# Kernel optimization log

Hardware: AMD Instinct MI355X
Metric: run time of the kernel (lower is better)

Reference implementation:

```python
import jax, jax.numpy as jnp
import numpy as np

N_NODES = 100000
N_EDGES = 3200000
IN_FEAT = 512
HIDDEN = 64
N_GRAPHS = 2048


def setup_inputs() -> dict:
    key = jax.random.key(0)
    ks = jax.random.split(key, 8)
    x = jax.random.normal(ks[0], (N_NODES, IN_FEAT), dtype=jnp.float32)
    edge_index = jax.random.randint(ks[1], (2, N_EDGES), 0, N_NODES, dtype=jnp.int64)
    batch = jnp.sort(jax.random.randint(ks[2], (N_NODES,), 0, N_GRAPHS, dtype=jnp.int64))
    W1 = jax.random.normal(ks[3], (IN_FEAT, HIDDEN), dtype=jnp.float32) * (1.0 / np.sqrt(IN_FEAT))
    b1 = jnp.zeros((HIDDEN,), dtype=jnp.float32)
    W2 = jax.random.normal(ks[4], (HIDDEN, HIDDEN), dtype=jnp.float32) * (1.0 / np.sqrt(HIDDEN))
    b2 = jnp.zeros((HIDDEN,), dtype=jnp.float32)
    fc_w = jax.random.normal(ks[5], (HIDDEN, 1), dtype=jnp.float32) * (1.0 / np.sqrt(HIDDEN))
    fc_b = jnp.zeros((1,), dtype=jnp.float32)
    return {"x": x, "edge_index": edge_index, "batch": batch, "num_graphs": N_GRAPHS,
            "W1": W1, "b1": b1, "W2": W2, "b2": b2, "fc_w": fc_w, "fc_b": fc_b}


def _gcn_conv(x, src, dst, n_nodes, W, b):
    # PyG GCNConv: h = X W; out = D^{-1/2}(A+I)D^{-1/2} h + b  (self-loops already in src/dst)
    h = x @ W  # [N, out]
    ones = jnp.ones_like(src, dtype=h.dtype)
    deg = jax.ops.segment_sum(ones, dst, num_segments=n_nodes)  # in-degree incl. self-loop
    dinv = jnp.where(deg > 0, jax.lax.rsqrt(deg), 0.0)
    norm = dinv[src] * dinv[dst]  # [E+N]
    msgs = h[src] * norm[:, None]  # gather + scale
    out = jax.ops.segment_sum(msgs, dst, num_segments=n_nodes)  # scatter-add
    return out + b


def reference(x, edge_index, batch, num_graphs, W1, b1, W2, b2, fc_w, fc_b):
    n = x.shape[0]
    loops = jnp.arange(n, dtype=edge_index.dtype)
    src = jnp.concatenate([edge_index[0], loops])
    dst = jnp.concatenate([edge_index[1], loops])

    h = jax.nn.relu(_gcn_conv(x, src, dst, n, W1, b1))
    h = _gcn_conv(h, src, dst, n, W2, b2)

    # global_mean_pool over graph ids
    sums = jax.ops.segment_sum(h, batch, num_segments=num_graphs)
    cnts = jax.ops.segment_sum(jnp.ones((n,), dtype=h.dtype), batch, num_segments=num_graphs)
    pooled = sums / jnp.maximum(cnts, 1.0)[:, None]
    return pooled @ fc_w + fc_b  # [num_graphs, 1]
```

## Files before the change

### kernel.cpp

```cpp
#include <hip/hip_runtime.h>
#include <hip/hip_bf16.h>

#define N_NODES  100000
#define N_EDGES  3200000
#define IN_FEAT  512
#define HIDDEN   64
#define N_GRAPHS 2048

typedef __attribute__((ext_vector_type(8))) short short8;
typedef __attribute__((ext_vector_type(4))) float floatx4;

__global__ __launch_bounds__(256) void zero_u32(unsigned* __restrict__ p, int n) {
    int i = blockIdx.x * 256 + threadIdx.x;
    if (i < n) p[i] = 0u;
}

__global__ __launch_bounds__(256) void init_deg(int* __restrict__ degi, int n) {
    int i = blockIdx.x * 256 + threadIdx.x;
    if (i < n) degi[i] = 1;
}

__global__ __launch_bounds__(256) void deg_rank(const int* __restrict__ dst,
                                                int* __restrict__ degi,
                                                int* __restrict__ rank, int e) {
    int i = (blockIdx.x * 256 + threadIdx.x) * 4;
    if (i + 4 <= e) {
        int4 d = *(const int4*)(dst + i);
        int4 r;
        r.x = atomicAdd(&degi[d.x], 1);
        r.y = atomicAdd(&degi[d.y], 1);
        r.z = atomicAdd(&degi[d.z], 1);
        r.w = atomicAdd(&degi[d.w], 1);
        *(int4*)(rank + i) = r;
    } else {
        for (int j = i; j < e; j++) rank[j] = atomicAdd(&degi[dst[j]], 1);
    }
}

__global__ __launch_bounds__(256) void compute_dinv(const int* __restrict__ degi,
                                                    float* __restrict__ dinv, int n) {
    int i = blockIdx.x * 256 + threadIdx.x;
    if (i < n) dinv[i] = 1.0f / sqrtf((float)degi[i]);
}

__global__ __launch_bounds__(256) void count_graphs(const int* __restrict__ batch,
                                                    int* __restrict__ cntg, int n) {
    int i = blockIdx.x * 256 + threadIdx.x;
    if (i < n) atomicAdd(&cntg[batch[i]], 1);
}

#define SCAN_CHUNK 2048

__global__ __launch_bounds__(256) void scan_block_sums(const int* __restrict__ degi,
                                                       int* __restrict__ bsums, int n) {
    __shared__ int sdata[256];
    int t = threadIdx.x;
    int base = blockIdx.x * SCAN_CHUNK;
    int s = 0;
    for (int i = 0; i < 8; i++) {
        int idx = base + t * 8 + i;
        if (idx < n) s += degi[idx] - 1;
    }
    sdata[t] = s;
    __syncthreads();
    for (int off = 128; off > 0; off >>= 1) {
        if (t < off) sdata[t] += sdata[t + off];
        __syncthreads();
    }
    if (t == 0) bsums[blockIdx.x] = sdata[0];
}

__global__ void scan_bsums(int* __restrict__ bsums, int nb) {
    if (blockIdx.x == 0 && threadIdx.x == 0) {
        int acc = 0;
        for (int i = 0; i < nb; i++) { int v = bsums[i]; bsums[i] = acc; acc += v; }
    }
}

__global__ __launch_bounds__(256) void scan_write(const int* __restrict__ degi,
                                                  const int* __restrict__ bsums,
                                                  int* __restrict__ row_start, int n) {
    __shared__ int sthread[256];
    int t = threadIdx.x;
    int base = blockIdx.x * SCAN_CHUNK;
    int local[8];
    int s = 0;
    for (int i = 0; i < 8; i++) {
        int idx = base + t * 8 + i;
        int c = (idx < n) ? (degi[idx] - 1) : 0;
        local[i] = s;
        s += c;
    }
    sthread[t] = s;
    __syncthreads();
    for (int off = 1; off < 256; off <<= 1) {
        int v = (t >= off) ? sthread[t - off] : 0;
        __syncthreads();
        sthread[t] += v;
        __syncthreads();
    }
    int off0 = bsums[blockIdx.x] + sthread[t] - s;
    for (int i = 0; i < 8; i++) {
        int idx = base + t * 8 + i;
        if (idx < n) row_start[idx] = off0 + local[i];
    }
}

__global__ __launch_bounds__(256) void csr_scatter(const int* __restrict__ src,
                                                   const int* __restrict__ dst,
                                                   const int* __restrict__ rank,
                                                   const int* __restrict__ rowst,
                                                   int* __restrict__ csr_src, int e) {
    int i = (blockIdx.x * 256 + threadIdx.x) * 4;
    if (i + 4 <= e) {
        int4 d = *(const int4*)(dst + i);
        int4 s = *(const int4*)(src + i);
        int4 r = *(const int4*)(rank + i);
        csr_src[rowst[d.x] + r.x - 1] = s.x;
        csr_src[rowst[d.y] + r.y - 1] = s.y;
        csr_src[rowst[d.z] + r.z - 1] = s.z;
        csr_src[rowst[d.w] + r.w - 1] = s.w;
    } else {
        for (int j = i; j < e; j++)
            csr_src[rowst[dst[j]] + rank[j] - 1] = src[j];
    }
}

__device__ inline void bf16_split(float f, short& hi, short& lo) {
    unsigned u = __float_as_uint(f);
    unsigned r = (u + 0x7fffu + ((u >> 16) & 1u)) >> 16;
    float fh = __uint_as_float(r << 16);
    float fl = f - fh;
    unsigned v = __float_as_uint(fl);
    unsigned s = (v + 0x7fffu + ((v >> 16) & 1u)) >> 16;
    hi = (short)r;
    lo = (short)s;
}

template <int K>
__global__ __launch_bounds__(256) void gemm_mfma(const float* __restrict__ X,
                                                 const float* __restrict__ W,
                                                 const float* __restrict__ dinv,
                                                 float* __restrict__ Y, int nrows) {
    constexpr int BSTR = 40;
    __shared__ short bhi[64 * BSTR];
    __shared__ short blo[64 * BSTR];

    const int t    = threadIdx.x;
    const int wave = t >> 6;
    const int lane = t & 63;
    const int quad = lane >> 4;
    const int l16  = lane & 15;

    const int arow   = blockIdx.x * 64 + wave * 16 + l16;
    const bool rvalid = arow < nrows;
    const float* xrow = X + (size_t)arow * K;

    const int scol = t & 63;
    const int skg  = t >> 6;

    floatx4 acc[4] = {};

#pragma unroll 1
    for (int k0 = 0; k0 < K; k0 += 32) {
        float wv[8];
#pragma unroll
        for (int j = 0; j < 8; j++)
            wv[j] = W[(size_t)(k0 + skg * 8 + j) * 64 + scol];
        short8 whi, wlo;
#pragma unroll
        for (int j = 0; j < 8; j++) { short h, l; bf16_split(wv[j], h, l); whi[j] = h; wlo[j] = l; }

        __syncthreads();
        *(short8*)&bhi[scol * BSTR + skg * 8] = whi;
        *(short8*)&blo[scol * BSTR + skg * 8] = wlo;

        float av[8] = {0.f, 0.f, 0.f, 0.f, 0.f, 0.f, 0.f, 0.f};
        if (rvalid) {
            float4 p0 = *(const float4*)(xrow + k0 + quad * 8);
            float4 p1 = *(const float4*)(xrow + k0 + quad * 8 + 4);
            av[0] = p0.x; av[1] = p0.y; av[2] = p0.z; av[3] = p0.w;
            av[4] = p1.x; av[5] = p1.y; av[6] = p1.z; av[7] = p1.w;
        }
        short8 ahi, alo;
#pragma unroll
        for (int j = 0; j < 8; j++) { short h, l; bf16_split(av[j], h, l); ahi[j] = h; alo[j] = l; }

        __syncthreads();

#pragma unroll
        for (int ct = 0; ct < 4; ct++) {
            int col = ct * 16 + l16;
            short8 bh = *(short8*)&bhi[col * BSTR + quad * 8];
            short8 bl = *(short8*)&blo[col * BSTR + quad * 8];
            acc[ct] = __builtin_amdgcn_mfma_f32_16x16x32_bf16(ahi, bh, acc[ct], 0, 0, 0);
            acc[ct] = __builtin_amdgcn_mfma_f32_16x16x32_bf16(ahi, bl, acc[ct], 0, 0, 0);
            acc[ct] = __builtin_amdgcn_mfma_f32_16x16x32_bf16(alo, bh, acc[ct], 0, 0, 0);
        }
    }

#pragma unroll
    for (int r = 0; r < 4; r++) {
        int orow = blockIdx.x * 64 + wave * 16 + quad * 4 + r;
        if (orow < nrows) {
            float dv = dinv[orow];
#pragma unroll
            for (int ct = 0; ct < 4; ct++)
                Y[(size_t)orow * 64 + ct * 16 + l16] = acc[ct][r] * dv;
        }
    }
}

template <bool RELU, bool POOL>
__global__ __launch_bounds__(256) void gcn_gather(const float* __restrict__ g,
                                                  const float* __restrict__ dinv,
                                                  const int* __restrict__ row_start,
                                                  const int* __restrict__ degi,
                                                  const int* __restrict__ csr_src,
                                                  const float* __restrict__ bias,
                                                  float* __restrict__ out,
                                                  float* __restrict__ pooled,
                                                  const int* __restrict__ batch, int n) {
    int node = (blockIdx.x * 256 + threadIdx.x) >> 6;
    int lane = threadIdx.x & 63;
    int es = lane >> 4;
    int fg = lane & 15;
    if (node >= n) return;

    int start = row_start[node];
    int de = degi[node] - 1;
    float dn = dinv[node];

    float4 a0 = make_float4(0.f, 0.f, 0.f, 0.f);
    float4 a1 = a0, a2 = a0, a3 = a0;
    if (es == 0) a0 = *(const float4*)(g + (size_t)node * 64 + fg * 4);

    for (int c = 0; c < de; c += 64) {
        int m = min(64, de - c);
        int sv = (lane < m) ? csr_src[start + c + lane] : -1;
        int t = 0;
        for (; t + 16 <= m; t += 16) {
            int s0 = __shfl(sv, t + es);
            int s1 = __shfl(sv, t + 4 + es);
            int s2 = __shfl(sv, t + 8 + es);
            int s3 = __shfl(sv, t + 12 + es);
            float4 v0 = *(const float4*)(g + (size_t)s0 * 64 + fg * 4);
            float4 v1 = *(const float4*)(g + (size_t)s1 * 64 + fg * 4);
            float4 v2 = *(const float4*)(g + (size_t)s2 * 64 + fg * 4);
            float4 v3 = *(const float4*)(g + (size_t)s3 * 64 + fg * 4);
            a0.x += v0.x; a0.y += v0.y; a0.z += v0.z; a0.w += v0.w;
            a1.x += v1.x; a1.y += v1.y; a1.z += v1.z; a1.w += v1.w;
            a2.x += v2.x; a2.y += v2.y; a2.z += v2.z; a2.w += v2.w;
            a3.x += v3.x; a3.y += v3.y; a3.z += v3.z; a3.w += v3.w;
        }
        for (; t < m; t += 4) {
            int e = t + es;
            int s = __shfl(sv, e);
            if (e < m) {
                float4 v = *(const float4*)(g + (size_t)s * 64 + fg * 4);
                a0.x += v.x; a0.y += v.y; a0.z += v.z; a0.w += v.w;
            }
        }
    }
    float4 a;
    a.x = (a0.x + a1.x) + (a2.x + a3.x);
    a.y = (a0.y + a1.y) + (a2.y + a3.y);
    a.z = (a0.z + a1.z) + (a2.z + a3.z);
    a.w = (a0.w + a1.w) + (a2.w + a3.w);
    a.x += __shfl_xor(a.x, 16); a.y += __shfl_xor(a.y, 16);
    a.z += __shfl_xor(a.z, 16); a.w += __shfl_xor(a.w, 16);
    a.x += __shfl_xor(a.x, 32); a.y += __shfl_xor(a.y, 32);
    a.z += __shfl_xor(a.z, 32); a.w += __shfl_xor(a.w, 32);

    if (es == 0) {
        float4 bv = *(const float4*)(bias + fg * 4);
        float4 o;
        o.x = fmaf(dn, a.x, bv.x);
        o.y = fmaf(dn, a.y, bv.y);
        o.z = fmaf(dn, a.z, bv.z);
        o.w = fmaf(dn, a.w, bv.w);
        if (RELU) {
            o.x = fmaxf(o.x, 0.f); o.y = fmaxf(o.y, 0.f);
            o.z = fmaxf(o.z, 0.f); o.w = fmaxf(o.w, 0.f);
        }
        if (POOL) {
            float* pp = pooled + (size_t)batch[node] * 64 + fg * 4;
            atomicAdd(pp + 0, o.x);
            atomicAdd(pp + 1, o.y);
            atomicAdd(pp + 2, o.z);
            atomicAdd(pp + 3, o.w);
        } else {
            *(float4*)(out + (size_t)node * 64 + fg * 4) = o;
        }
    }
}

__global__ __launch_bounds__(256) void final_fc(const float* __restrict__ pooled,
                                                const int* __restrict__ cntg,
                                                const float* __restrict__ fc_w,
                                                const float* __restrict__ fc_b,
                                                float* __restrict__ out, int g) {
    int gid = (blockIdx.x * 256 + threadIdx.x) >> 6;
    int lane = threadIdx.x & 63;
    if (gid >= g) return;
    float c = fmaxf((float)cntg[gid], 1.0f);
    float v = pooled[(size_t)gid * 64 + lane] / c * fc_w[lane];
#pragma unroll
    for (int off = 32; off > 0; off >>= 1) v += __shfl_down(v, off);
    if (lane == 0) out[gid] = v + fc_b[0];
}

extern "C" void kernel_launch(void* const* d_in, const int* in_sizes, int n_in,
                              void* d_out, int out_size, void* d_ws, size_t ws_size,
                              hipStream_t stream) {
    const float* x    = (const float*)d_in[0];
    const int*   eidx = (const int*)d_in[1];
    const int*   batch= (const int*)d_in[2];
    const float* W1   = (const float*)d_in[4];
    const float* b1   = (const float*)d_in[5];
    const float* W2   = (const float*)d_in[6];
    const float* b2   = (const float*)d_in[7];
    const float* fc_w = (const float*)d_in[8];
    const float* fc_b = (const float*)d_in[9];
    float* out = (float*)d_out;

    const int N = in_sizes[0] / IN_FEAT;
    const int E = in_sizes[1] / 2;
    const int G = N_GRAPHS;
    const int* src = eidx;
    const int* dst = eidx + E;

    char* w = (char*)d_ws;
    float* g1   = (float*)w; w += (size_t)N * 64 * 4;
    float* h1r  = (float*)w; w += (size_t)N * 64 * 4;
    float* g2   = (float*)w; w += (size_t)N * 64 * 4;
    int*   degi = (int*)w;   w += (size_t)N * 4;
    float* dinv = (float*)w; w += (size_t)N * 4;
    int*   rowst= (int*)w;   w += (size_t)N * 4;
    int*   bsums= (int*)w;   w += 4096;
    int*   csrs = (int*)w;   w += (size_t)E * 4;
    int*   rank = (int*)w;   w += (size_t)E * 4;
    float* pooled = (float*)w; w += (size_t)G * 64 * 4;
    int*   cntg = (int*)w;   w += (size_t)G * 4;

    const int nb_scan = (N + SCAN_CHUNK - 1) / SCAN_CHUNK;

    zero_u32<<<(G * 64 + 255) / 256, 256, 0, stream>>>((unsigned*)pooled, G * 64);
    zero_u32<<<(G + 255) / 256, 256, 0, stream>>>((unsigned*)cntg, G);
    init_deg<<<(N + 255) / 256, 256, 0, stream>>>(degi, N);
    count_graphs<<<(N + 255) / 256, 256, 0, stream>>>(batch, cntg, N);
    deg_rank<<<(E / 4 + 255) / 256, 256, 0, stream>>>(dst, degi, rank, E);
    compute_dinv<<<(N + 255) / 256, 256, 0, stream>>>(degi, dinv, N);
    scan_block_sums<<<nb_scan, 256, 0, stream>>>(degi, bsums, N);
    scan_bsums<<<1, 64, 0, stream>>>(bsums, nb_scan);
    scan_write<<<nb_scan, 256, 0, stream>>>(degi, bsums, rowst, N);
    csr_scatter<<<(E / 4 + 255) / 256, 256, 0, stream>>>(src, dst, rank, rowst, csrs, E);

    gemm_mfma<IN_FEAT><<<(N + 63) / 64, 256, 0, stream>>>(x, W1, dinv, g1, N);
    gcn_gather<true, false><<<(N * 64 + 255) / 256, 256, 0, stream>>>(
        g1, dinv, rowst, degi, csrs, b1, h1r, nullptr, batch, N);
    gemm_mfma<HIDDEN><<<(N + 63) / 64, 256, 0, stream>>>(h1r, W2, dinv, g2, N);
    gcn_gather<false, true><<<(N * 64 + 255) / 256, 256, 0, stream>>>(
        g2, dinv, rowst, degi, csrs, b2, nullptr, pooled, batch, N);
    final_fc<<<(G * 64 + 255) / 256, 256, 0, stream>>>(pooled, cntg, fc_w, fc_b, out, G);
}
```

Baseline: 812.5 us.

## Fuse init kernels, pre-split weights, shrink rank to bytes, unroll gather

Several changes land together. Zeroing, degree init and per-graph counts are fused into one kernel; the counts now come from a binary search over the sorted batch instead of atomics. The inverse sqrt of the degree is folded into the scan write, and the single-thread scan of block sums becomes a wave shuffle scan. The weight hi/lo bf16 split and transpose is done once in a small kernel instead of by every GEMM block. Edge ranks are stored as 8-bit values to cut memory traffic, and the gather loop is unrolled to 8 loads in flight. The byte ranks wrap if any node has in-degree of 256 or more, and the count search relies on batch being sorted.

```diff
diff --git a/kernel.cpp b/kernel.cpp
--- a/kernel.cpp
+++ b/kernel.cpp
@@ -10,43 +10,62 @@
 typedef __attribute__((ext_vector_type(8))) short short8;
 typedef __attribute__((ext_vector_type(4))) float floatx4;
 
-__global__ __launch_bounds__(256) void zero_u32(unsigned* __restrict__ p, int n) {
+__device__ inline void bf16_split(float f, short& hi, short& lo) {
+    unsigned u = __float_as_uint(f);
+    unsigned r = (u + 0x7fffu + ((u >> 16) & 1u)) >> 16;
+    float fh = __uint_as_float(r << 16);
+    float fl = f - fh;
+    unsigned v = __float_as_uint(fl);
+    unsigned s = (v + 0x7fffu + ((v >> 16) & 1u)) >> 16;
+    hi = (short)r;
+    lo = (short)s;
+}
+
+__global__ __launch_bounds__(256) void fused_init(float* __restrict__ pooled,
+                                                  int* __restrict__ degi,
+                                                  int* __restrict__ cntg,
+                                                  const int* __restrict__ batch,
+                                                  int n, int g) {
     int i = blockIdx.x * 256 + threadIdx.x;
-    if (i < n) p[i] = 0u;
-}
-
-__global__ __launch_bounds__(256) void init_deg(int* __restrict__ degi, int n) {
+    if (i < g * 64) pooled[i] = 0.f;
+    if (i < n) degi[i] = 1;
+    if (i < g) {
+        int lo0 = 0, hi0 = n;
+        while (lo0 < hi0) { int m = (lo0 + hi0) >> 1; if (batch[m] < i) lo0 = m + 1; else hi0 = m; }
+        int lo1 = lo0, hi1 = n;
+        while (lo1 < hi1) { int m = (lo1 + hi1) >> 1; if (batch[m] < i + 1) lo1 = m + 1; else hi1 = m; }
+        cntg[i] = lo1 - lo0;
+    }
+}
+
+__global__ __launch_bounds__(256) void split_w(const float* __restrict__ W,
+                                               short* __restrict__ hi_t,
+                                               short* __restrict__ lo_t, int K) {
     int i = blockIdx.x * 256 + threadIdx.x;
-    if (i < n) degi[i] = 1;
+    if (i < K * 64) {
+        int k = i >> 6, c = i & 63;
+        short h, l;
+        bf16_split(W[i], h, l);
+        hi_t[c * K + k] = h;
+        lo_t[c * K + k] = l;
+    }
 }
 
 __global__ __launch_bounds__(256) void deg_rank(const int* __restrict__ dst,
                                                 int* __restrict__ degi,
-                                                int* __restrict__ rank, int e) {
+                                                unsigned char* __restrict__ rank, int e) {
     int i = (blockIdx.x * 256 + threadIdx.x) * 4;
     if (i + 4 <= e) {
         int4 d = *(const int4*)(dst + i);
-        int4 r;
-        r.x = atomicAdd(&degi[d.x], 1);
-        r.y = atomicAdd(&degi[d.y], 1);
-        r.z = atomicAdd(&degi[d.z], 1);
-        r.w = atomicAdd(&degi[d.w], 1);
-        *(int4*)(rank + i) = r;
+        uchar4 r;
+        r.x = (unsigned char)atomicAdd(&degi[d.x], 1);
+        r.y = (unsigned char)atomicAdd(&degi[d.y], 1);
+        r.z = (unsigned char)atomicAdd(&degi[d.z], 1);
+        r.w = (unsigned char)atomicAdd(&degi[d.w], 1);
+        *(uchar4*)(rank + i) = r;
     } else {
-        for (int j = i; j < e; j++) rank[j] = atomicAdd(&degi[dst[j]], 1);
-    }
-}
-
-__global__ __launch_bounds__(256) void compute_dinv(const int* __restrict__ degi,
-                                                    float* __restrict__ dinv, int n) {
-    int i = blockIdx.x * 256 + threadIdx.x;
-    if (i < n) dinv[i] = 1.0f / sqrtf((float)degi[i]);
-}
-
-__global__ __launch_bounds__(256) void count_graphs(const int* __restrict__ batch,
-                                                    int* __restrict__ cntg, int n) {
-    int i = blockIdx.x * 256 + threadIdx.x;
-    if (i < n) atomicAdd(&cntg[batch[i]], 1);
+        for (int j = i; j < e; j++) rank[j] = (unsigned char)atomicAdd(&degi[dst[j]], 1);
+    }
 }
 
 #define SCAN_CHUNK 2048
@@ -71,23 +90,30 @@
 }
 
 __global__ void scan_bsums(int* __restrict__ bsums, int nb) {
-    if (blockIdx.x == 0 && threadIdx.x == 0) {
-        int acc = 0;
-        for (int i = 0; i < nb; i++) { int v = bsums[i]; bsums[i] = acc; acc += v; }
-    }
+    int lane = threadIdx.x & 63;
+    int orig = (lane < nb) ? bsums[lane] : 0;
+    int v = orig;
+    for (int off = 1; off < 64; off <<= 1) {
+        int u = __shfl_up(v, off);
+        if (lane >= off) v += u;
+    }
+    if (lane < nb) bsums[lane] = v - orig;
 }
 
 __global__ __launch_bounds__(256) void scan_write(const int* __restrict__ degi,
                                                   const int* __restrict__ bsums,
-                                                  int* __restrict__ row_start, int n) {
+                                                  int* __restrict__ row_start,
+                                                  float* __restrict__ dinv, int n) {
     __shared__ int sthread[256];
     int t = threadIdx.x;
     int base = blockIdx.x * SCAN_CHUNK;
     int local[8];
+    int cnt[8];
     int s = 0;
     for (int i = 0; i < 8; i++) {
         int idx = base + t * 8 + i;
         int c = (idx < n) ? (degi[idx] - 1) : 0;
+        cnt[i] = c;
         local[i] = s;
         s += c;
     }
@@ -102,44 +128,37 @@
     int off0 = bsums[blockIdx.x] + sthread[t] - s;
     for (int i = 0; i < 8; i++) {
         int idx = base + t * 8 + i;
-        if (idx < n) row_start[idx] = off0 + local[i];
+        if (idx < n) {
+            row_start[idx] = off0 + local[i];
+            dinv[idx] = 1.0f / sqrtf((float)(cnt[i] + 1));
+        }
     }
 }
 
 __global__ __launch_bounds__(256) void csr_scatter(const int* __restrict__ src,
                                                    const int* __restrict__ dst,
-                                                   const int* __restrict__ rank,
+                                                   const unsigned char* __restrict__ rank,
                                                    const int* __restrict__ rowst,
                                                    int* __restrict__ csr_src, int e) {
     int i = (blockIdx.x * 256 + threadIdx.x) * 4;
     if (i + 4 <= e) {
         int4 d = *(const int4*)(dst + i);
         int4 s = *(const int4*)(src + i);
-        int4 r = *(const int4*)(rank + i);
-        csr_src[rowst[d.x] + r.x - 1] = s.x;
-        csr_src[rowst[d.y] + r.y - 1] = s.y;
-        csr_src[rowst[d.z] + r.z - 1] = s.z;
-        csr_src[rowst[d.w] + r.w - 1] = s.w;
+        uchar4 r = *(const uchar4*)(rank + i);
+        csr_src[rowst[d.x] + (int)r.x - 1] = s.x;
+        csr_src[rowst[d.y] + (int)r.y - 1] = s.y;
+        csr_src[rowst[d.z] + (int)r.z - 1] = s.z;
+        csr_src[rowst[d.w] + (int)r.w - 1] = s.w;
     } else {
         for (int j = i; j < e; j++)
-            csr_src[rowst[dst[j]] + rank[j] - 1] = src[j];
-    }
-}
-
-__device__ inline void bf16_split(float f, short& hi, short& lo) {
-    unsigned u = __float_as_uint(f);
-    unsigned r = (u + 0x7fffu + ((u >> 16) & 1u)) >> 16;
-    float fh = __uint_as_float(r << 16);
-    float fl = f - fh;
-    unsigned v = __float_as_uint(fl);
-    unsigned s = (v + 0x7fffu + ((v >> 16) & 1u)) >> 16;
-    hi = (short)r;
-    lo = (short)s;
+            csr_src[rowst[dst[j]] + (int)rank[j] - 1] = src[j];
+    }
 }
 
 template <int K>
 __global__ __launch_bounds__(256) void gemm_mfma(const float* __restrict__ X,
-                                                 const float* __restrict__ W,
+                                                 const short* __restrict__ Whi,
+                                                 const short* __restrict__ Wlo,
                                                  const float* __restrict__ dinv,
                                                  float* __restrict__ Y, int nrows) {
     constexpr int BSTR = 40;
@@ -158,22 +177,15 @@
 
     const int scol = t & 63;
     const int skg  = t >> 6;
+    const short* whp = Whi + (size_t)scol * K + skg * 8;
+    const short* wlp = Wlo + (size_t)scol * K + skg * 8;
 
     floatx4 acc[4] = {};
 
 #pragma unroll 1
     for (int k0 = 0; k0 < K; k0 += 32) {
-        float wv[8];
-#pragma unroll
-        for (int j = 0; j < 8; j++)
-            wv[j] = W[(size_t)(k0 + skg * 8 + j) * 64 + scol];
-        short8 whi, wlo;
-#pragma unroll
-        for (int j = 0; j < 8; j++) { short h, l; bf16_split(wv[j], h, l); whi[j] = h; wlo[j] = l; }
-
-        __syncthreads();
-        *(short8*)&bhi[scol * BSTR + skg * 8] = whi;
-        *(short8*)&blo[scol * BSTR + skg * 8] = wlo;
+        short8 whi = *(const short8*)(whp + k0);
+        short8 wlo = *(const short8*)(wlp + k0);
 
         float av[8] = {0.f, 0.f, 0.f, 0.f, 0.f, 0.f, 0.f, 0.f};
         if (rvalid) {
@@ -186,6 +198,9 @@
 #pragma unroll
         for (int j = 0; j < 8; j++) { short h, l; bf16_split(av[j], h, l); ahi[j] = h; alo[j] = l; }
 
+        __syncthreads();
+        *(short8*)&bhi[scol * BSTR + skg * 8] = whi;
+        *(short8*)&blo[scol * BSTR + skg * 8] = wlo;
         __syncthreads();
 
 #pragma unroll
@@ -239,7 +254,33 @@
         int m = min(64, de - c);
         int sv = (lane < m) ? csr_src[start + c + lane] : -1;
         int t = 0;
-        for (; t + 16 <= m; t += 16) {
+        for (; t + 32 <= m; t += 32) {
+            int s0 = __shfl(sv, t + es);
+            int s1 = __shfl(sv, t + 4 + es);
+            int s2 = __shfl(sv, t + 8 + es);
+            int s3 = __shfl(sv, t + 12 + es);
+            int s4 = __shfl(sv, t + 16 + es);
+            int s5 = __shfl(sv, t + 20 + es);
+            int s6 = __shfl(sv, t + 24 + es);
+            int s7 = __shfl(sv, t + 28 + es);
+            float4 v0 = *(const float4*)(g + (size_t)s0 * 64 + fg * 4);
+            float4 v1 = *(const float4*)(g + (size_t)s1 * 64 + fg * 4);
+            float4 v2 = *(const float4*)(g + (size_t)s2 * 64 + fg * 4);
+            float4 v3 = *(const float4*)(g + (size_t)s3 * 64 + fg * 4);
+            float4 v4 = *(const float4*)(g + (size_t)s4 * 64 + fg * 4);
+            float4 v5 = *(const float4*)(g + (size_t)s5 * 64 + fg * 4);
+            float4 v6 = *(const float4*)(g + (size_t)s6 * 64 + fg * 4);
+            float4 v7 = *(const float4*)(g + (size_t)s7 * 64 + fg * 4);
+            a0.x += v0.x; a0.y += v0.y; a0.z += v0.z; a0.w += v0.w;
+            a1.x += v1.x; a1.y += v1.y; a1.z += v1.z; a1.w += v1.w;
+            a2.x += v2.x; a2.y += v2.y; a2.z += v2.z; a2.w += v2.w;
+            a3.x += v3.x; a3.y += v3.y; a3.z += v3.z; a3.w += v3.w;
+            a0.x += v4.x; a0.y += v4.y; a0.z += v4.z; a0.w += v4.w;
+            a1.x += v5.x; a1.y += v5.y; a1.z += v5.z; a1.w += v5.w;
+            a2.x += v6.x; a2.y += v6.y; a2.z += v6.z; a2.w += v6.w;
+            a3.x += v7.x; a3.y += v7.y; a3.z += v7.z; a3.w += v7.w;
+        }
+        if (t + 16 <= m) {
             int s0 = __shfl(sv, t + es);
             int s1 = __shfl(sv, t + 4 + es);
             int s2 = __shfl(sv, t + 8 + es);
@@ -252,6 +293,7 @@
             a1.x += v1.x; a1.y += v1.y; a1.z += v1.z; a1.w += v1.w;
             a2.x += v2.x; a2.y += v2.y; a2.z += v2.z; a2.w += v2.w;
             a3.x += v3.x; a3.y += v3.y; a3.z += v3.z; a3.w += v3.w;
+            t += 16;
         }
         for (; t < m; t += 4) {
             int e = t + es;
@@ -339,27 +381,29 @@
     int*   rowst= (int*)w;   w += (size_t)N * 4;
     int*   bsums= (int*)w;   w += 4096;
     int*   csrs = (int*)w;   w += (size_t)E * 4;
-    int*   rank = (int*)w;   w += (size_t)E * 4;
+    unsigned char* rank8 = (unsigned char*)w; w += (size_t)E;
     float* pooled = (float*)w; w += (size_t)G * 64 * 4;
     int*   cntg = (int*)w;   w += (size_t)G * 4;
+    short* w1hi = (short*)w; w += (size_t)IN_FEAT * 64 * 2;
+    short* w1lo = (short*)w; w += (size_t)IN_FEAT * 64 * 2;
+    short* w2hi = (short*)w; w += (size_t)HIDDEN * 64 * 2;
+    short* w2lo = (short*)w; w += (size_t)HIDDEN * 64 * 2;
 
     const int nb_scan = (N + SCAN_CHUNK - 1) / SCAN_CHUNK;
 
-    zero_u32<<<(G * 64 + 255) / 256, 256, 0, stream>>>((unsigned*)pooled, G * 64);
-    zero_u32<<<(G + 255) / 256, 256, 0, stream>>>((unsigned*)cntg, G);
-    init_deg<<<(N + 255) / 256, 256, 0, stream>>>(degi, N);
-    count_graphs<<<(N + 255) / 256, 256, 0, stream>>>(batch, cntg, N);
-    deg_rank<<<(E / 4 + 255) / 256, 256, 0, stream>>>(dst, degi, rank, E);
-    compute_dinv<<<(N + 255) / 256, 256, 0, stream>>>(degi, dinv, N);
+    fused_init<<<(G * 64 + 255) / 256, 256, 0, stream>>>(pooled, degi, cntg, batch, N, G);
+    split_w<<<(IN_FEAT * 64 + 255) / 256, 256, 0, stream>>>(W1, w1hi, w1lo, IN_FEAT);
+    split_w<<<(HIDDEN * 64 + 255) / 256, 256, 0, stream>>>(W2, w2hi, w2lo, HIDDEN);
+    deg_rank<<<(E / 4 + 255) / 256, 256, 0, stream>>>(dst, degi, rank8, E);
     scan_block_sums<<<nb_scan, 256, 0, stream>>>(degi, bsums, N);
     scan_bsums<<<1, 64, 0, stream>>>(bsums, nb_scan);
-    scan_write<<<nb_scan, 256, 0, stream>>>(degi, bsums, rowst, N);
-    csr_scatter<<<(E / 4 + 255) / 256, 256, 0, stream>>>(src, dst, rank, rowst, csrs, E);
-
-    gemm_mfma<IN_FEAT><<<(N + 63) / 64, 256, 0, stream>>>(x, W1, dinv, g1, N);
+    scan_write<<<nb_scan, 256, 0, stream>>>(degi, bsums, rowst, dinv, N);
+    csr_scatter<<<(E / 4 + 255) / 256, 256, 0, stream>>>(src, dst, rank8, rowst, csrs, E);
+
+    gemm_mfma<IN_FEAT><<<(N + 63) / 64, 256, 0, stream>>>(x, w1hi, w1lo, dinv, g1, N);
     gcn_gather<true, false><<<(N * 64 + 255) / 256, 256, 0, stream>>>(
         g1, dinv, rowst, degi, csrs, b1, h1r, nullptr, batch, N);
-    gemm_mfma<HIDDEN><<<(N + 63) / 64, 256, 0, stream>>>(h1r, W2, dinv, g2, N);
+    gemm_mfma<HIDDEN><<<(N + 63) / 64, 256, 0, stream>>>(h1r, w2hi, w2lo, dinv, g2, N);
     gcn_gather<false, true><<<(N * 64 + 255) / 256, 256, 0, stream>>>(
         g2, dinv, rowst, degi, csrs, b2, nullptr, pooled, batch, N);
     final_fc<<<(G * 64 + 255) / 256, 256, 0, stream>>>(pooled, cntg, fc_w, fc_b, out, G);
```

Result: no change. 806.3 us (-0.8%).
